# Performance work log

Hardware: AMD Instinct MI355X
Metric: run time of the kernel (lower is better)

Reference implementation:

```python
import jax, jax.numpy as jnp
import numpy as np

B, N, E = 4, 8192, 1024
H, G = 16, 64            # num_heads, num_groups
D = E // H               # head_dim = 64
GS = N // G              # group (block) size = 128


def setup_inputs() -> dict:
    key = jax.random.key(0)
    ks = jax.random.split(key, 11)
    std = 0.02
    mk = lambda k, shape: (jax.random.normal(k, shape, dtype=jnp.float32) * std)
    return {
        "q": jax.random.normal(ks[0], (B, N, E), dtype=jnp.float32),
        "k": jax.random.normal(ks[1], (B, N, E), dtype=jnp.float32),
        "v": jax.random.normal(ks[2], (B, N, E), dtype=jnp.float32),
        "Wq": mk(ks[3], (E, E)), "bq": jnp.zeros((E,), jnp.float32),
        "Wk": mk(ks[4], (E, E)), "bk": jnp.zeros((E,), jnp.float32),
        "Wv": mk(ks[5], (E, E)), "bv": jnp.zeros((E,), jnp.float32),
        "Wo": mk(ks[6], (E, E)), "bo": jnp.zeros((E,), jnp.float32),
    }


def reference(q, k, v, Wq, bq, Wk, bk, Wv, bv, Wo, bo):
    b, n, e = q.shape
    scale = 1.0 / (D ** 0.5)

    def proj(x, W, bias):
        # [b,n,e] -> [b,H,G,GS,D]  (split heads, then split seq into groups)
        y = x @ W + bias
        return y.reshape(b, n, H, D).transpose(0, 2, 1, 3).reshape(b, H, G, GS, D)

    qh = proj(q, Wq, bq)
    kh = proj(k, Wk, bk)
    vh = proj(v, Wv, bv)

    # block-diagonal attention: each seq group attends only within itself
    scores = jnp.einsum('bhgqd,bhgkd->bhgqk', qh, kh) * scale  # [b,H,G,GS,GS]
    w = jax.nn.softmax(scores, axis=-1)
    og = jnp.einsum('bhgqk,bhgkd->bhgqd', w, vh)               # [b,H,G,GS,D]

    out = og.reshape(b, H, n, D).transpose(0, 2, 1, 3).reshape(b, n, e)
    out = out @ Wo + bo
    # torch version returns attn_weights of the last group from the loop
    return out, w[:, :, -1]
```

## Files before the change

### kernel.cpp

```cpp
#include <hip/hip_runtime.h>
#include <stdint.h>

#define DEVI static __device__ __forceinline__

typedef __attribute__((ext_vector_type(8))) __bf16 bf16x8;
typedef __attribute__((ext_vector_type(4))) float f32x4;

#define MFMA16(a, b, c) __builtin_amdgcn_mfma_f32_16x16x32_bf16((a), (b), (c), 0, 0, 0)

DEVI uint16_t f2bf(float f) {
  uint32_t u = __builtin_bit_cast(uint32_t, f);
  u += 0x7fffu + ((u >> 16) & 1u);
  return (uint16_t)(u >> 16);
}

DEVI void gload16(const void* g, void* l) {
  __builtin_amdgcn_global_load_lds((const __attribute__((address_space(1))) void*)g,
                                   (__attribute__((address_space(3))) void*)l, 16, 0, 0);
}

#define BARRIER()                         \
  do {                                    \
    __builtin_amdgcn_sched_barrier(0);    \
    __builtin_amdgcn_s_barrier();         \
    __builtin_amdgcn_sched_barrier(0);    \
  } while (0)

#define LGKM0_FENCE()                                      \
  do {                                                     \
    asm volatile("s_waitcnt lgkmcnt(0)" ::: "memory");     \
    __builtin_amdgcn_sched_barrier(0);                     \
  } while (0)

__global__ __launch_bounds__(256) void cvt_bf16(const float* __restrict__ in,
                                                uint16_t* __restrict__ out, long n) {
  long i = ((long)blockIdx.x * 256 + threadIdx.x) * 8;
  if (i >= n) return;
  float4 a = *(const float4*)(in + i);
  float4 b = *(const float4*)(in + i + 4);
  union { uint16_t u[8]; uint4 v; } r;
  r.u[0] = f2bf(a.x); r.u[1] = f2bf(a.y); r.u[2] = f2bf(a.z); r.u[3] = f2bf(a.w);
  r.u[4] = f2bf(b.x); r.u[5] = f2bf(b.y); r.u[6] = f2bf(b.z); r.u[7] = f2bf(b.w);
  *(uint4*)(out + i) = r.v;
}

struct W4 {
  const float* W[4];
  uint16_t* Wt[4];
};

__global__ __launch_bounds__(256) void wtrans4(W4 p) {
  __shared__ float t[64][65];
  const float* __restrict__ W = p.W[blockIdx.z];
  uint16_t* __restrict__ Wt = p.Wt[blockIdx.z];
  const int ti = blockIdx.y * 64, tj = blockIdx.x * 64;
  {
    int r = threadIdx.x >> 2, c0 = (threadIdx.x & 3) * 16;
#pragma unroll
    for (int i = 0; i < 16; i += 4) {
      float4 v = *(const float4*)(W + (size_t)(ti + r) * 1024 + tj + c0 + i);
      t[r][c0 + i + 0] = v.x; t[r][c0 + i + 1] = v.y;
      t[r][c0 + i + 2] = v.z; t[r][c0 + i + 3] = v.w;
    }
  }
  __syncthreads();
  {
    int c = threadIdx.x >> 2, r0 = (threadIdx.x & 3) * 16;
    union { uint16_t u[16]; uint4 v[2]; } b;
#pragma unroll
    for (int i = 0; i < 16; ++i) b.u[i] = f2bf(t[r0 + i][c]);
    uint16_t* dst = Wt + (size_t)(tj + c) * 1024 + ti + r0;
    *(uint4*)dst = b.v[0];
    *(uint4*)(dst + 8) = b.v[1];
  }
}

__global__ __launch_bounds__(256, 3) void gemm128(const uint16_t* __restrict__ A,
                                                  const uint16_t* __restrict__ Bt,
                                                  const float* __restrict__ bias,
                                                  void* __restrict__ C, int cf32) {
  __shared__ uint8_t lds[49152];
  const int tid = threadIdx.x;
  const int l = tid & 63, w = tid >> 6;
  const int wr = w >> 1, wc = w & 1;
  const int lc = l & 15, lq = l >> 4;

  const int bid = blockIdx.y * 8 + blockIdx.x;
  const int swz = (bid & 7) * 256 + (bid >> 3);
  const size_t m0 = (size_t)(swz >> 3) * 128;
  const int n0 = (swz & 7) * 128;

  const uint8_t* Ab = (const uint8_t*)A + m0 * 2048;
  const uint8_t* Bb = (const uint8_t*)Bt + (size_t)n0 * 2048;

  const int lrow = l >> 3;
  const int susw = ((l & 7) ^ lrow) * 16;

  auto stageA = [&](int buf, int kt) {
#pragma unroll
    for (int j = 0; j < 4; ++j) {
      const int c = w * 4 + j;
      gload16(Ab + (size_t)(c * 8 + lrow) * 2048 + kt * 128 + susw,
              lds + buf * 16384 + c * 1024);
    }
  };
  auto stageB = [&](int kt) {
#pragma unroll
    for (int j = 0; j < 4; ++j) {
      const int c = w * 4 + j;
      gload16(Bb + (size_t)(c * 8 + lrow) * 2048 + kt * 128 + susw,
              lds + 32768 + c * 1024);
    }
  };

  auto ldsA = [&](int buf, int mi, int kk) -> bf16x8 {
    const int row = wr * 64 + mi * 16 + lc;
    const int u = ((kk * 4 + lq) ^ (row & 7)) * 16;
    return *(const bf16x8*)(lds + buf * 16384 + row * 128 + u);
  };
  auto ldsB = [&](int ni, int kk) -> bf16x8 {
    const int row = wc * 64 + ni * 16 + lc;
    const int u = ((kk * 4 + lq) ^ (row & 7)) * 16;
    return *(const bf16x8*)(lds + 32768 + row * 128 + u);
  };

  f32x4 acc[4][4] = {};

  stageA(0, 0);
  stageB(0);
  asm volatile("s_waitcnt vmcnt(0)" ::: "memory");
  BARRIER();

  for (int t = 0; t < 16; ++t) {
    const int cur = t & 1;
    const bool more = (t + 1 < 16);

    bf16x8 bF[4][2];
#pragma unroll
    for (int ni = 0; ni < 4; ++ni)
#pragma unroll
      for (int kk = 0; kk < 2; ++kk) bF[ni][kk] = ldsB(ni, kk);
    LGKM0_FENCE();
    BARRIER();

    if (more) {
      stageB(t + 1);
      stageA(cur ^ 1, t + 1);
    }

#pragma unroll
    for (int kk = 0; kk < 2; ++kk) {
      bf16x8 aF[4];
#pragma unroll
      for (int mi = 0; mi < 4; ++mi) aF[mi] = ldsA(cur, mi, kk);
      __builtin_amdgcn_s_setprio(1);
#pragma unroll
      for (int mi = 0; mi < 4; ++mi)
#pragma unroll
        for (int ni = 0; ni < 4; ++ni)
          acc[mi][ni] = MFMA16(aF[mi], bF[ni][kk], acc[mi][ni]);
      __builtin_amdgcn_s_setprio(0);
    }

    if (more) {
      asm volatile("s_waitcnt vmcnt(0)" ::: "memory");
      BARRIER();
    }
  }

#pragma unroll
  for (int mi = 0; mi < 4; ++mi) {
#pragma unroll
    for (int ni = 0; ni < 4; ++ni) {
      const int col = n0 + wc * 64 + ni * 16 + lc;
      const float bb = bias[col];
#pragma unroll
      for (int r = 0; r < 4; ++r) {
        const size_t row = m0 + wr * 64 + mi * 16 + lq * 4 + r;
        const float vv = acc[mi][ni][r] + bb;
        if (cf32) ((float*)C)[row * 1024 + col] = vv;
        else      ((uint16_t*)C)[row * 1024 + col] = f2bf(vv);
      }
    }
  }
}

__global__ __launch_bounds__(256) void attn(const uint16_t* __restrict__ Qh,
                                            const uint16_t* __restrict__ Kh,
                                            const uint16_t* __restrict__ Vh,
                                            uint16_t* __restrict__ Oh,
                                            float* __restrict__ Wlast) {
  __shared__ uint16_t Ks[128][72];
  __shared__ uint16_t Vt[64][136];
  __shared__ uint16_t Ps[128][136];

  const int blk = blockIdx.x;
  const int b = blk >> 10;
  const int h = (blk >> 6) & 15;
  const int g = blk & 63;
  const size_t rowbase = (size_t)b * 8192 + (size_t)g * 128;
  const int colbase = h * 64;

  const int tid = threadIdx.x, lane = tid & 63, wv = tid >> 6;
  const int lc = lane & 15, lq = lane >> 4;
  const int m0 = wv * 32;

  {
    const int r = tid >> 1, hf = (tid & 1) * 32;
    const uint16_t* ksrc = Kh + (rowbase + r) * 1024 + colbase + hf;
    const uint16_t* vsrc = Vh + (rowbase + r) * 1024 + colbase + hf;
    union { uint16_t u[32]; uint4 v[4]; } kk, vb;
#pragma unroll
    for (int i = 0; i < 4; ++i) kk.v[i] = *(const uint4*)(ksrc + i * 8);
#pragma unroll
    for (int i = 0; i < 4; ++i) vb.v[i] = *(const uint4*)(vsrc + i * 8);
#pragma unroll
    for (int i = 0; i < 4; ++i) *(uint4*)&Ks[r][hf + i * 8] = kk.v[i];
#pragma unroll
    for (int j = 0; j < 32; ++j) Vt[hf + j][r] = vb.u[j];
  }

  bf16x8 aq[2][2];
#pragma unroll
  for (int mi = 0; mi < 2; ++mi)
#pragma unroll
    for (int ks = 0; ks < 2; ++ks)
      aq[mi][ks] = *(const bf16x8*)(Qh + (rowbase + m0 + mi * 16 + lc) * 1024 +
                                    colbase + ks * 32 + lq * 8);

  __syncthreads();

  f32x4 sacc[2][8] = {};
#pragma unroll
  for (int ks = 0; ks < 2; ++ks) {
#pragma unroll
    for (int ni = 0; ni < 8; ++ni) {
      bf16x8 bk = *(const bf16x8*)&Ks[ni * 16 + lc][ks * 32 + lq * 8];
      sacc[0][ni] = MFMA16(aq[0][ks], bk, sacc[0][ni]);
      sacc[1][ni] = MFMA16(aq[1][ks], bk, sacc[1][ni]);
    }
  }

  const float scale = 0.125f;
  float mx[2][4], sm[2][4];
#pragma unroll
  for (int mi = 0; mi < 2; ++mi)
#pragma unroll
    for (int r = 0; r < 4; ++r) {
      float m = -1e30f;
#pragma unroll
      for (int ni = 0; ni < 8; ++ni) m = fmaxf(m, sacc[mi][ni][r]);
      m = fmaxf(m, __shfl_xor(m, 1));
      m = fmaxf(m, __shfl_xor(m, 2));
      m = fmaxf(m, __shfl_xor(m, 4));
      m = fmaxf(m, __shfl_xor(m, 8));
      mx[mi][r] = m * scale;
    }
#pragma unroll
  for (int mi = 0; mi < 2; ++mi)
#pragma unroll
    for (int ni = 0; ni < 8; ++ni)
#pragma unroll
      for (int r = 0; r < 4; ++r)
        sacc[mi][ni][r] = __expf(sacc[mi][ni][r] * scale - mx[mi][r]);
#pragma unroll
  for (int mi = 0; mi < 2; ++mi)
#pragma unroll
    for (int r = 0; r < 4; ++r) {
      float s = 0.f;
#pragma unroll
      for (int ni = 0; ni < 8; ++ni) s += sacc[mi][ni][r];
      s += __shfl_xor(s, 1); s += __shfl_xor(s, 2);
      s += __shfl_xor(s, 4); s += __shfl_xor(s, 8);
      sm[mi][r] = 1.0f / s;
    }

#pragma unroll
  for (int mi = 0; mi < 2; ++mi)
#pragma unroll
    for (int ni = 0; ni < 8; ++ni)
#pragma unroll
      for (int r = 0; r < 4; ++r) {
        float wgt = sacc[mi][ni][r] * sm[mi][r];
        sacc[mi][ni][r] = wgt;
        Ps[m0 + mi * 16 + lq * 4 + r][ni * 16 + lc] = f2bf(wgt);
      }
  if (g == 63) {
    float* wl = Wlast + (size_t)(b * 16 + h) * 16384;
#pragma unroll
    for (int mi = 0; mi < 2; ++mi)
#pragma unroll
      for (int ni = 0; ni < 8; ++ni)
#pragma unroll
        for (int r = 0; r < 4; ++r)
          wl[(size_t)(m0 + mi * 16 + lq * 4 + r) * 128 + ni * 16 + lc] =
              sacc[mi][ni][r];
  }
  __syncthreads();

  f32x4 oacc[2][4] = {};
#pragma unroll
  for (int ks = 0; ks < 4; ++ks) {
    bf16x8 ap[2], bq[4];
#pragma unroll
    for (int mi = 0; mi < 2; ++mi)
      ap[mi] = *(const bf16x8*)&Ps[m0 + mi * 16 + lc][ks * 32 + lq * 8];
#pragma unroll
    for (int ni = 0; ni < 4; ++ni)
      bq[ni] = *(const bf16x8*)&Vt[ni * 16 + lc][ks * 32 + lq * 8];
#pragma unroll
    for (int mi = 0; mi < 2; ++mi)
#pragma unroll
      for (int ni = 0; ni < 4; ++ni)
        oacc[mi][ni] = MFMA16(ap[mi], bq[ni], oacc[mi][ni]);
  }
#pragma unroll
  for (int mi = 0; mi < 2; ++mi)
#pragma unroll
    for (int ni = 0; ni < 4; ++ni)
#pragma unroll
      for (int r = 0; r < 4; ++r)
        Oh[(rowbase + m0 + mi * 16 + lq * 4 + r) * 1024 + colbase + ni * 16 + lc] =
            f2bf(oacc[mi][ni][r]);
}

extern "C" void kernel_launch(void* const* d_in, const int* in_sizes, int n_in,
                              void* d_out, int out_size, void* d_ws, size_t ws_size,
                              hipStream_t stream) {
  (void)in_sizes; (void)n_in; (void)out_size; (void)ws_size;
  const float* q  = (const float*)d_in[0];
  const float* k  = (const float*)d_in[1];
  const float* v  = (const float*)d_in[2];
  const float* Wq = (const float*)d_in[3];
  const float* bq = (const float*)d_in[4];
  const float* Wk = (const float*)d_in[5];
  const float* bk = (const float*)d_in[6];
  const float* Wv = (const float*)d_in[7];
  const float* bv = (const float*)d_in[8];
  const float* Wo = (const float*)d_in[9];
  const float* bo = (const float*)d_in[10];

  uint8_t* ws = (uint8_t*)d_ws;
  const size_t WSZ = (size_t)1024 * 1024 * 2;
  const size_t TSZ = (size_t)32768 * 1024 * 2;
  uint16_t* Wtq = (uint16_t*)(ws + 0 * WSZ);
  uint16_t* Wtk = (uint16_t*)(ws + 1 * WSZ);
  uint16_t* Wtv = (uint16_t*)(ws + 2 * WSZ);
  uint16_t* Wto = (uint16_t*)(ws + 3 * WSZ);
  uint16_t* Qh  = (uint16_t*)(ws + 4 * WSZ);
  uint16_t* Khp = (uint16_t*)(ws + 4 * WSZ + 1 * TSZ);
  uint16_t* Vhp = (uint16_t*)(ws + 4 * WSZ + 2 * TSZ);
  uint16_t* Xs  = (uint16_t*)(ws + 4 * WSZ + 3 * TSZ);

  W4 wt;
  wt.W[0] = Wq; wt.W[1] = Wk; wt.W[2] = Wv; wt.W[3] = Wo;
  wt.Wt[0] = Wtq; wt.Wt[1] = Wtk; wt.Wt[2] = Wtv; wt.Wt[3] = Wto;
  wtrans4<<<dim3(16, 16, 4), 256, 0, stream>>>(wt);

  const long NE = (long)32768 * 1024;
  const dim3 gg(8, 256), gb(256);
  cvt_bf16<<<16384, 256, 0, stream>>>(q, Xs, NE);
  gemm128<<<gg, gb, 0, stream>>>(Xs, Wtq, bq, Qh, 0);
  cvt_bf16<<<16384, 256, 0, stream>>>(k, Xs, NE);
  gemm128<<<gg, gb, 0, stream>>>(Xs, Wtk, bk, Khp, 0);
  cvt_bf16<<<16384, 256, 0, stream>>>(v, Xs, NE);
  gemm128<<<gg, gb, 0, stream>>>(Xs, Wtv, bv, Vhp, 0);

  float* outp = (float*)d_out;
  attn<<<4096, 256, 0, stream>>>(Qh, Khp, Vhp, Xs, outp + (size_t)32768 * 1024);
  gemm128<<<gg, gb, 0, stream>>>(Xs, Wto, bo, outp, 1);
}
```

Before: 467.7 us.

## Fuse fp32-to-bf16 input conversion into projection GEMM A-tile loading

Removes the three standalone cvt_bf16 passes over the q/k/v activations. The projection GEMM now loads fp32 A tiles into registers, converts them to bf16 and writes them into swizzled LDS, replacing the direct global-to-LDS path. This avoids writing and re-reading a 64MB bf16 intermediate per projection. In exchange the GEMM reads twice as many A bytes, each A tile is fetched by all 8 column blocks, and the loop uses more registers plus an extra LDS-write/wait step.

```diff
diff --git a/kernel.cpp b/kernel.cpp
--- a/kernel.cpp
+++ b/kernel.cpp
@@ -31,18 +31,6 @@
     asm volatile("s_waitcnt lgkmcnt(0)" ::: "memory");     \
     __builtin_amdgcn_sched_barrier(0);                     \
   } while (0)
-
-__global__ __launch_bounds__(256) void cvt_bf16(const float* __restrict__ in,
-                                                uint16_t* __restrict__ out, long n) {
-  long i = ((long)blockIdx.x * 256 + threadIdx.x) * 8;
-  if (i >= n) return;
-  float4 a = *(const float4*)(in + i);
-  float4 b = *(const float4*)(in + i + 4);
-  union { uint16_t u[8]; uint4 v; } r;
-  r.u[0] = f2bf(a.x); r.u[1] = f2bf(a.y); r.u[2] = f2bf(a.z); r.u[3] = f2bf(a.w);
-  r.u[4] = f2bf(b.x); r.u[5] = f2bf(b.y); r.u[6] = f2bf(b.z); r.u[7] = f2bf(b.w);
-  *(uint4*)(out + i) = r.v;
-}
 
 struct W4 {
   const float* W[4];
@@ -75,7 +63,8 @@
   }
 }
 
-__global__ __launch_bounds__(256, 3) void gemm128(const uint16_t* __restrict__ A,
+template <int AF32>
+__global__ __launch_bounds__(256, 3) void gemm128(const void* __restrict__ Ap,
                                                   const uint16_t* __restrict__ Bt,
                                                   const float* __restrict__ bias,
                                                   void* __restrict__ C, int cf32) {
@@ -90,13 +79,14 @@
   const size_t m0 = (size_t)(swz >> 3) * 128;
   const int n0 = (swz & 7) * 128;
 
-  const uint8_t* Ab = (const uint8_t*)A + m0 * 2048;
+  const float* Af = (const float*)Ap;
+  const uint8_t* Ab = (const uint8_t*)Ap + m0 * 2048;
   const uint8_t* Bb = (const uint8_t*)Bt + (size_t)n0 * 2048;
 
   const int lrow = l >> 3;
   const int susw = ((l & 7) ^ lrow) * 16;
 
-  auto stageA = [&](int buf, int kt) {
+  auto stageA_bf = [&](int buf, int kt) {
 #pragma unroll
     for (int j = 0; j < 4; ++j) {
       const int c = w * 4 + j;
@@ -113,6 +103,26 @@
     }
   };
 
+  auto loadA = [&](int kt, float4 (&ra)[8]) {
+#pragma unroll
+    for (int j = 0; j < 8; ++j) {
+      const int row = w * 32 + j * 4 + (l >> 4);
+      ra[j] = *(const float4*)(Af + (m0 + row) * 1024 + kt * 64 + (l & 15) * 4);
+    }
+  };
+  auto writeA = [&](int buf, const float4 (&ra)[8]) {
+#pragma unroll
+    for (int j = 0; j < 8; ++j) {
+      const int row = w * 32 + j * 4 + (l >> 4);
+      const int u = (l & 15) >> 1;
+      union { uint16_t h[4]; uint2 v; } tv;
+      tv.h[0] = f2bf(ra[j].x); tv.h[1] = f2bf(ra[j].y);
+      tv.h[2] = f2bf(ra[j].z); tv.h[3] = f2bf(ra[j].w);
+      *(uint2*)(lds + buf * 16384 + row * 128 + ((u ^ (row & 7)) << 4) +
+                (l & 1) * 8) = tv.v;
+    }
+  };
+
   auto ldsA = [&](int buf, int mi, int kk) -> bf16x8 {
     const int row = wr * 64 + mi * 16 + lc;
     const int u = ((kk * 4 + lq) ^ (row & 7)) * 16;
@@ -126,9 +136,18 @@
 
   f32x4 acc[4][4] = {};
 
-  stageA(0, 0);
-  stageB(0);
-  asm volatile("s_waitcnt vmcnt(0)" ::: "memory");
+  if constexpr (AF32) {
+    float4 r0[8];
+    loadA(0, r0);
+    stageB(0);
+    writeA(0, r0);
+    asm volatile("s_waitcnt vmcnt(0)" ::: "memory");
+    LGKM0_FENCE();
+  } else {
+    stageA_bf(0, 0);
+    stageB(0);
+    asm volatile("s_waitcnt vmcnt(0)" ::: "memory");
+  }
   BARRIER();
 
   for (int t = 0; t < 16; ++t) {
@@ -143,9 +162,11 @@
     LGKM0_FENCE();
     BARRIER();
 
+    float4 ra[8];
     if (more) {
       stageB(t + 1);
-      stageA(cur ^ 1, t + 1);
+      if constexpr (AF32) loadA(t + 1, ra);
+      else                stageA_bf(cur ^ 1, t + 1);
     }
 
 #pragma unroll
@@ -163,7 +184,9 @@
     }
 
     if (more) {
+      if constexpr (AF32) writeA(cur ^ 1, ra);
       asm volatile("s_waitcnt vmcnt(0)" ::: "memory");
+      LGKM0_FENCE();
       BARRIER();
     }
   }
@@ -357,16 +380,12 @@
   wt.Wt[0] = Wtq; wt.Wt[1] = Wtk; wt.Wt[2] = Wtv; wt.Wt[3] = Wto;
   wtrans4<<<dim3(16, 16, 4), 256, 0, stream>>>(wt);
 
-  const long NE = (long)32768 * 1024;
   const dim3 gg(8, 256), gb(256);
-  cvt_bf16<<<16384, 256, 0, stream>>>(q, Xs, NE);
-  gemm128<<<gg, gb, 0, stream>>>(Xs, Wtq, bq, Qh, 0);
-  cvt_bf16<<<16384, 256, 0, stream>>>(k, Xs, NE);
-  gemm128<<<gg, gb, 0, stream>>>(Xs, Wtk, bk, Khp, 0);
-  cvt_bf16<<<16384, 256, 0, stream>>>(v, Xs, NE);
-  gemm128<<<gg, gb, 0, stream>>>(Xs, Wtv, bv, Vhp, 0);
+  gemm128<1><<<gg, gb, 0, stream>>>(q, Wtq, bq, Qh, 0);
+  gemm128<1><<<gg, gb, 0, stream>>>(k, Wtk, bk, Khp, 0);
+  gemm128<1><<<gg, gb, 0, stream>>>(v, Wtv, bv, Vhp, 0);
 
   float* outp = (float*)d_out;
   attn<<<4096, 256, 0, stream>>>(Qh, Khp, Vhp, Xs, outp + (size_t)32768 * 1024);
-  gemm128<<<gg, gb, 0, stream>>>(Xs, Wto, bo, outp, 1);
-}
+  gemm128<0><<<gg, gb, 0, stream>>>(Xs, Wto, bo, outp, 1);
+}
```

After: 702.3 us. 1.5x slower.

## Load GEMM B operand directly from global into registers, dropping its LDS staging

Applied to the files above, without the earlier changes.

The B (weight) tile is no longer staged through LDS; each lane reads its bf16x8 B fragments straight from global memory each k-step. This removes one barrier and the lgkmcnt fence per iteration and cuts LDS use from 48KB to 32KB, which may allow more resident blocks. In exchange, B loads are no longer shared across waves through LDS, so global/L2 traffic for B rises, and load latency sits directly in front of the MFMAs with no prefetch.

```diff
diff --git a/kernel.cpp b/kernel.cpp
--- a/kernel.cpp
+++ b/kernel.cpp
@@ -24,12 +24,6 @@
     __builtin_amdgcn_sched_barrier(0);    \
     __builtin_amdgcn_s_barrier();         \
     __builtin_amdgcn_sched_barrier(0);    \
-  } while (0)
-
-#define LGKM0_FENCE()                                      \
-  do {                                                     \
-    asm volatile("s_waitcnt lgkmcnt(0)" ::: "memory");     \
-    __builtin_amdgcn_sched_barrier(0);                     \
   } while (0)
 
 __global__ __launch_bounds__(256) void cvt_bf16(const float* __restrict__ in,
@@ -79,7 +73,7 @@
                                                   const uint16_t* __restrict__ Bt,
                                                   const float* __restrict__ bias,
                                                   void* __restrict__ C, int cf32) {
-  __shared__ uint8_t lds[49152];
+  __shared__ uint8_t lds[32768];
   const int tid = threadIdx.x;
   const int l = tid & 63, w = tid >> 6;
   const int wr = w >> 1, wc = w & 1;
@@ -91,7 +85,6 @@
   const int n0 = (swz & 7) * 128;
 
   const uint8_t* Ab = (const uint8_t*)A + m0 * 2048;
-  const uint8_t* Bb = (const uint8_t*)Bt + (size_t)n0 * 2048;
 
   const int lrow = l >> 3;
   const int susw = ((l & 7) ^ lrow) * 16;
@@ -102,14 +95,6 @@
       const int c = w * 4 + j;
       gload16(Ab + (size_t)(c * 8 + lrow) * 2048 + kt * 128 + susw,
               lds + buf * 16384 + c * 1024);
-    }
-  };
-  auto stageB = [&](int kt) {
-#pragma unroll
-    for (int j = 0; j < 4; ++j) {
-      const int c = w * 4 + j;
-      gload16(Bb + (size_t)(c * 8 + lrow) * 2048 + kt * 128 + susw,
-              lds + 32768 + c * 1024);
     }
   };
 
@@ -118,16 +103,15 @@
     const int u = ((kk * 4 + lq) ^ (row & 7)) * 16;
     return *(const bf16x8*)(lds + buf * 16384 + row * 128 + u);
   };
-  auto ldsB = [&](int ni, int kk) -> bf16x8 {
-    const int row = wc * 64 + ni * 16 + lc;
-    const int u = ((kk * 4 + lq) ^ (row & 7)) * 16;
-    return *(const bf16x8*)(lds + 32768 + row * 128 + u);
+
+  const uint16_t* Bw = Bt + (size_t)(n0 + wc * 64 + lc) * 1024 + lq * 8;
+  auto loadB = [&](int kt, int ni, int kk) -> bf16x8 {
+    return *(const bf16x8*)(Bw + (size_t)ni * 16 * 1024 + kt * 64 + kk * 32);
   };
 
   f32x4 acc[4][4] = {};
 
   stageA(0, 0);
-  stageB(0);
   asm volatile("s_waitcnt vmcnt(0)" ::: "memory");
   BARRIER();
 
@@ -139,14 +123,8 @@
 #pragma unroll
     for (int ni = 0; ni < 4; ++ni)
 #pragma unroll
-      for (int kk = 0; kk < 2; ++kk) bF[ni][kk] = ldsB(ni, kk);
-    LGKM0_FENCE();
-    BARRIER();
-
-    if (more) {
-      stageB(t + 1);
-      stageA(cur ^ 1, t + 1);
-    }
+      for (int kk = 0; kk < 2; ++kk) bF[ni][kk] = loadB(t, ni, kk);
+    if (more) stageA(cur ^ 1, t + 1);
 
 #pragma unroll
     for (int kk = 0; kk < 2; ++kk) {
```

Measured after the change: 745.0 us. 1.59x slower.

## Halve GEMM K-tile to raise occupancy and stage bf16 epilogues through LDS

Applied to the files above, without the earlier changes.

The GEMM K-tile drops from 64 to 32 elements per stage, which halves LDS use to 24KB and raises the launch-bounds occupancy target from 3 to 5 blocks per CU, at the cost of twice as many loop iterations and barriers. The LDS swizzle is reworked for the narrower 64-byte rows. The bf16 GEMM output and the attention output are now staged through LDS and written with coalesced 16-byte stores instead of scattered 2-byte stores. The extra synchronisation and the shorter MFMA bursts per barrier may offset the gains from higher occupancy.

```diff
diff --git a/kernel.cpp b/kernel.cpp
--- a/kernel.cpp
+++ b/kernel.cpp
@@ -75,11 +75,11 @@
   }
 }
 
-__global__ __launch_bounds__(256, 3) void gemm128(const uint16_t* __restrict__ A,
+__global__ __launch_bounds__(256, 5) void gemm128(const uint16_t* __restrict__ A,
                                                   const uint16_t* __restrict__ Bt,
                                                   const float* __restrict__ bias,
                                                   void* __restrict__ C, int cf32) {
-  __shared__ uint8_t lds[49152];
+  __shared__ uint8_t lds[24576];
   const int tid = threadIdx.x;
   const int l = tid & 63, w = tid >> 6;
   const int wr = w >> 1, wc = w & 1;
@@ -93,35 +93,34 @@
   const uint8_t* Ab = (const uint8_t*)A + m0 * 2048;
   const uint8_t* Bb = (const uint8_t*)Bt + (size_t)n0 * 2048;
 
-  const int lrow = l >> 3;
-  const int susw = ((l & 7) ^ lrow) * 16;
+  const int srow_in = l >> 2;
+  const int sug = (((l & 3) ^ ((l >> 4) & 3))) * 16;
 
   auto stageA = [&](int buf, int kt) {
 #pragma unroll
-    for (int j = 0; j < 4; ++j) {
-      const int c = w * 4 + j;
-      gload16(Ab + (size_t)(c * 8 + lrow) * 2048 + kt * 128 + susw,
-              lds + buf * 16384 + c * 1024);
+    for (int j = 0; j < 2; ++j) {
+      const int c = w * 2 + j;
+      gload16(Ab + (size_t)(c * 16 + srow_in) * 2048 + kt * 64 + sug,
+              lds + buf * 8192 + c * 1024);
     }
   };
   auto stageB = [&](int kt) {
 #pragma unroll
-    for (int j = 0; j < 4; ++j) {
-      const int c = w * 4 + j;
-      gload16(Bb + (size_t)(c * 8 + lrow) * 2048 + kt * 128 + susw,
-              lds + 32768 + c * 1024);
+    for (int j = 0; j < 2; ++j) {
+      const int c = w * 2 + j;
+      gload16(Bb + (size_t)(c * 16 + srow_in) * 2048 + kt * 64 + sug,
+              lds + 16384 + c * 1024);
     }
   };
 
-  auto ldsA = [&](int buf, int mi, int kk) -> bf16x8 {
+  const int ru = (lq ^ (lc >> 2)) * 16;
+  auto ldsA = [&](int buf, int mi) -> bf16x8 {
     const int row = wr * 64 + mi * 16 + lc;
-    const int u = ((kk * 4 + lq) ^ (row & 7)) * 16;
-    return *(const bf16x8*)(lds + buf * 16384 + row * 128 + u);
+    return *(const bf16x8*)(lds + buf * 8192 + row * 64 + ru);
   };
-  auto ldsB = [&](int ni, int kk) -> bf16x8 {
+  auto ldsB = [&](int ni) -> bf16x8 {
     const int row = wc * 64 + ni * 16 + lc;
-    const int u = ((kk * 4 + lq) ^ (row & 7)) * 16;
-    return *(const bf16x8*)(lds + 32768 + row * 128 + u);
+    return *(const bf16x8*)(lds + 16384 + row * 64 + ru);
   };
 
   f32x4 acc[4][4] = {};
@@ -131,15 +130,13 @@
   asm volatile("s_waitcnt vmcnt(0)" ::: "memory");
   BARRIER();
 
-  for (int t = 0; t < 16; ++t) {
+  for (int t = 0; t < 32; ++t) {
     const int cur = t & 1;
-    const bool more = (t + 1 < 16);
-
-    bf16x8 bF[4][2];
-#pragma unroll
-    for (int ni = 0; ni < 4; ++ni)
-#pragma unroll
-      for (int kk = 0; kk < 2; ++kk) bF[ni][kk] = ldsB(ni, kk);
+    const bool more = (t + 1 < 32);
+
+    bf16x8 bF[4];
+#pragma unroll
+    for (int ni = 0; ni < 4; ++ni) bF[ni] = ldsB(ni);
     LGKM0_FENCE();
     BARRIER();
 
@@ -148,19 +145,16 @@
       stageA(cur ^ 1, t + 1);
     }
 
-#pragma unroll
-    for (int kk = 0; kk < 2; ++kk) {
-      bf16x8 aF[4];
-#pragma unroll
-      for (int mi = 0; mi < 4; ++mi) aF[mi] = ldsA(cur, mi, kk);
-      __builtin_amdgcn_s_setprio(1);
-#pragma unroll
-      for (int mi = 0; mi < 4; ++mi)
-#pragma unroll
-        for (int ni = 0; ni < 4; ++ni)
-          acc[mi][ni] = MFMA16(aF[mi], bF[ni][kk], acc[mi][ni]);
-      __builtin_amdgcn_s_setprio(0);
-    }
+    bf16x8 aF[4];
+#pragma unroll
+    for (int mi = 0; mi < 4; ++mi) aF[mi] = ldsA(cur, mi);
+    __builtin_amdgcn_s_setprio(1);
+#pragma unroll
+    for (int mi = 0; mi < 4; ++mi)
+#pragma unroll
+      for (int ni = 0; ni < 4; ++ni)
+        acc[mi][ni] = MFMA16(aF[mi], bF[ni], acc[mi][ni]);
+    __builtin_amdgcn_s_setprio(0);
 
     if (more) {
       asm volatile("s_waitcnt vmcnt(0)" ::: "memory");
@@ -168,19 +162,48 @@
     }
   }
 
-#pragma unroll
-  for (int mi = 0; mi < 4; ++mi) {
-#pragma unroll
-    for (int ni = 0; ni < 4; ++ni) {
-      const int col = n0 + wc * 64 + ni * 16 + lc;
-      const float bb = bias[col];
-#pragma unroll
-      for (int r = 0; r < 4; ++r) {
-        const size_t row = m0 + wr * 64 + mi * 16 + lq * 4 + r;
-        const float vv = acc[mi][ni][r] + bb;
-        if (cf32) ((float*)C)[row * 1024 + col] = vv;
-        else      ((uint16_t*)C)[row * 1024 + col] = f2bf(vv);
+  if (cf32) {
+#pragma unroll
+    for (int mi = 0; mi < 4; ++mi)
+#pragma unroll
+      for (int ni = 0; ni < 4; ++ni) {
+        const int col = n0 + wc * 64 + ni * 16 + lc;
+        const float bb = bias[col];
+#pragma unroll
+        for (int r = 0; r < 4; ++r) {
+          const size_t row = m0 + wr * 64 + mi * 16 + lq * 4 + r;
+          ((float*)C)[row * 1024 + col] = acc[mi][ni][r] + bb;
+        }
       }
+  } else {
+    BARRIER();
+    uint16_t* st = (uint16_t*)lds;
+#pragma unroll
+    for (int ch = 0; ch < 2; ++ch) {
+#pragma unroll
+      for (int mi2 = 0; mi2 < 2; ++mi2) {
+        const int mi = ch * 2 + mi2;
+#pragma unroll
+        for (int ni = 0; ni < 4; ++ni) {
+          const int col = wc * 64 + ni * 16 + lc;
+          const float bb = bias[n0 + col];
+#pragma unroll
+          for (int r = 0; r < 4; ++r) {
+            const int prow = wr * 32 + mi2 * 16 + lq * 4 + r;
+            st[prow * 128 + col] = f2bf(acc[mi][ni][r] + bb);
+          }
+        }
+      }
+      __syncthreads();
+#pragma unroll
+      for (int i = 0; i < 4; ++i) {
+        const int p = (tid >> 4) + i * 16;
+        const int c16 = tid & 15;
+        const size_t grow = m0 + (p >> 5) * 64 + ch * 32 + (p & 31);
+        *(uint4*)((uint8_t*)C + grow * 2048 + n0 * 2 + c16 * 16) =
+            *(const uint4*)((const uint8_t*)st + p * 256 + c16 * 16);
+      }
+      if (ch == 0) __syncthreads();
     }
   }
 }
@@ -314,14 +337,23 @@
       for (int ni = 0; ni < 4; ++ni)
         oacc[mi][ni] = MFMA16(ap[mi], bq[ni], oacc[mi][ni]);
   }
+
+  uint16_t* os = &Ks[0][0];
 #pragma unroll
   for (int mi = 0; mi < 2; ++mi)
 #pragma unroll
     for (int ni = 0; ni < 4; ++ni)
 #pragma unroll
       for (int r = 0; r < 4; ++r)
-        Oh[(rowbase + m0 + mi * 16 + lq * 4 + r) * 1024 + colbase + ni * 16 + lc] =
-            f2bf(oacc[mi][ni][r]);
+        os[(m0 + mi * 16 + lq * 4 + r) * 64 + ni * 16 + lc] = f2bf(oacc[mi][ni][r]);
+  __syncthreads();
+#pragma unroll
+  for (int i = 0; i < 4; ++i) {
+    const int row = i * 32 + (tid >> 3);
+    const int c8 = tid & 7;
+    *(uint4*)(Oh + (rowbase + row) * 1024 + colbase + c8 * 8) =
+        *(const uint4*)(os + row * 64 + c8 * 8);
+  }
 }
 
 extern "C" void kernel_launch(void* const* d_in, const int* in_sizes, int n_in,
```

Measured after the change: 1.051 ms. +124.7%, slower.
